# Performance work log

Hardware: AMD Instinct MI355X
Metric: run time of the kernel (lower is better)

The kernel has to match this reference:

```python
import jax, jax.numpy as jnp
import numpy as np

B, T, C = 2, 2048, 2048
NH, HS = 16, 128          # heads, head_size = C // NH
NLQ, NLKV = 512, 512      # q / kv latent dims
DHR = 64                  # decoupled rope head dim


def _rope_cos_sin(T, dhr, dtype=jnp.float32):
    inv = 1.0 / (10000.0 ** (np.arange(0, dhr, 2, dtype=np.float32) / dhr))
    ang = np.arange(T, dtype=np.float32)[:, None] * inv[None, :]  # [T, dhr//2]
    return jnp.asarray(np.cos(ang), dtype), jnp.asarray(np.sin(ang), dtype)


def setup_inputs() -> dict:
    key = jax.random.key(0)
    ks = jax.random.split(key, 10)
    s = 0.02
    cos, sin = _rope_cos_sin(T, DHR)
    return {
        "x":     jax.random.normal(ks[0], (B, T, C), jnp.float32),
        "cos":   cos,
        "sin":   sin,
        "W_dq":  s * jax.random.normal(ks[1], (NLQ, C), jnp.float32),
        "W_uq":  s * jax.random.normal(ks[2], (C, NLQ), jnp.float32),
        "W_dkv": s * jax.random.normal(ks[3], (NLKV, C), jnp.float32),
        "W_uk":  s * jax.random.normal(ks[4], (C, NLKV), jnp.float32),
        "W_uv":  s * jax.random.normal(ks[5], (C, NLKV), jnp.float32),
        "W_qr":  s * jax.random.normal(ks[6], (NH * DHR, NLQ), jnp.float32),
        "W_kr":  s * jax.random.normal(ks[7], (DHR, C), jnp.float32),
        "W_o":   s * jax.random.normal(ks[8], (C, C), jnp.float32),
    }


def _apply_rope(x, cos, sin):
    # x: [B, T, H, D]; pairs are interleaved (even=real, odd=imag)
    xr = x.reshape(x.shape[:-1] + (-1, 2))
    re, im = xr[..., 0], xr[..., 1]
    c = cos[None, :, None, :]
    s = sin[None, :, None, :]
    out = jnp.stack([re * c - im * s, re * s + im * c], axis=-1)
    return out.reshape(x.shape)


def reference(x, cos, sin, W_dq, W_uq, W_dkv, W_uk, W_uv, W_qr, W_kr, W_o):
    b, t, c = x.shape
    nh, hs, nlq, nlkv, dhr = NH, HS, NLQ, NLKV, DHR
    scale = 1.0 / np.sqrt(hs + dhr).astype(np.float32)

    # low-rank latents
    c_q = x @ W_dq.T          # [B, T, nlq]
    c_kv = x @ W_dkv.T        # [B, T, nlkv]

    # absorbed matrices (training path)
    # W_uq: [C, nlq] viewed as [nlq, nh, hs]; W_uk: [C, nlkv] viewed as [nh, hs, nlkv]
    k_eff = jnp.einsum('qhd,hdk->hqk', W_uq.reshape(nlq, nh, hs),
                       W_uk.reshape(nh, hs, nlkv))              # [nh, nlq, nlkv]
    v_eff = (W_uv.T @ W_o.T).reshape(nlkv, nh, hs).transpose(1, 0, 2)  # [nh, nlkv, hs]

    # content scores via absorbed low-rank path
    qk = jnp.einsum('btq,hqk->bhtk', c_q, k_eff)                # [B, nh, T, nlkv]
    attn_c = jnp.einsum('bhtk,bsk->bhts', qk, c_kv)             # [B, nh, T, T]

    # decoupled RoPE scores
    c_kr = (x @ W_kr.T)[:, :, None, :]                          # [B, T, 1, dhr]
    k_r = _apply_rope(c_kr, cos, sin)[:, :, 0, :]               # [B, T, dhr]
    c_qr = (c_q @ W_qr.T).reshape(b, t, nh, dhr)
    q_r = _apply_rope(c_qr, cos, sin)                            # [B, T, nh, dhr]
    attn_r = jnp.einsum('bthd,bsd->bhts', q_r, k_r)             # [B, nh, T, T]

    attn = (attn_c + attn_r) * scale
    mask = jnp.tril(jnp.ones((t, t), dtype=bool))
    attn = jnp.where(mask[None, None], attn, -jnp.inf)
    p = jax.nn.softmax(attn, axis=-1)

    ctx = jnp.einsum('bhts,bsk->bhtk', p, c_kv)                 # [B, nh, T, nlkv]
    y = jnp.einsum('bhtk,hkd->bthd', ctx, v_eff).reshape(b, t, c)
    return y
```

## Files before the change

kernel.cpp:

```cpp
#include <hip/hip_runtime.h>
#include <hip/hip_bf16.h>
#include <math.h>

typedef long long ll;
typedef unsigned short ushort_t;
typedef __attribute__((ext_vector_type(8))) __bf16 bf16x8;
typedef __attribute__((ext_vector_type(4))) float f32x4;

__device__ __forceinline__ ushort_t f2bf(float f) {
    __hip_bfloat16 h = __float2bfloat16(f);
    return *reinterpret_cast<ushort_t*>(&h);
}
__device__ __forceinline__ float bf2f(ushort_t u) {
    return __uint_as_float(((unsigned)u) << 16);
}
__device__ __forceinline__ void stage16(const void* g_lane, void* lds_uniform) {
    __builtin_amdgcn_global_load_lds(
        (const __attribute__((address_space(1))) unsigned int*)g_lane,
        (__attribute__((address_space(3))) unsigned int*)lds_uniform, 16, 0, 0);
}

#define DPPMAX(v, ctrl) v = fmaxf(v, __uint_as_float((unsigned)__builtin_amdgcn_update_dpp( \
        0, (int)__float_as_uint(v), (ctrl), 0xF, 0xF, true)))
#define DPPADD(v, ctrl) v = v + __uint_as_float((unsigned)__builtin_amdgcn_update_dpp( \
        0, (int)__float_as_uint(v), (ctrl), 0xF, 0xF, true))
__device__ __forceinline__ float red_max16(float v) {
    DPPMAX(v, 0xB1); DPPMAX(v, 0x4E); DPPMAX(v, 0x141); DPPMAX(v, 0x140); return v;
}
__device__ __forceinline__ float red_sum16(float v) {
    DPPADD(v, 0xB1); DPPADD(v, 0x4E); DPPADD(v, 0x141); DPPADD(v, 0x140); return v;
}

#define TM 128
#define TN 128
#define TK 64

__global__ __launch_bounds__(256)
void gemm_bf16(const ushort_t* __restrict__ Ab, const ushort_t* __restrict__ Bb,
               void* __restrict__ Cb,
               int M, int N, int K,
               int a_rs, int b_rs, int c_rs, int Z2,
               ll a_bs1, ll a_bs2, ll b_bs1, ll b_bs2, ll c_bs1, ll c_bs2,
               int out_f32)
{
    const int m0 = blockIdx.y * TM;
    const int n0 = blockIdx.x * TN;
    const int z1 = blockIdx.z / Z2, z2 = blockIdx.z % Z2;

    const ushort_t* A = Ab + z1 * a_bs1 + z2 * a_bs2;
    const ushort_t* B = Bb + z1 * b_bs1 + z2 * b_bs2;

    __shared__ ushort_t As[2][TM][TK];
    __shared__ ushort_t Bs[2][TN][TK];

    const int tid  = threadIdx.x;
    const int w    = tid >> 6;
    const int l    = tid & 63;
    const int lo16 = l & 15;
    const int quad = l >> 4;
    const int wm0  = (w & 1) * 64;
    const int wn0  = (w >> 1) * 64;

    const int srow  = l >> 3;
    const int sunit = (l & 7) ^ srow;

    f32x4 acc[4][4];
    const f32x4 zero = {0.f, 0.f, 0.f, 0.f};
#pragma unroll
    for (int mi = 0; mi < 4; ++mi)
#pragma unroll
        for (int nj = 0; nj < 4; ++nj) acc[mi][nj] = zero;

    const int nIter = K / TK;

#pragma unroll
    for (int i = 0; i < 4; ++i) {
        const int rr = w * 32 + i * 8;
        stage16(A + (ll)(m0 + rr + srow) * a_rs + sunit * 8, &As[0][rr][0]);
        stage16(B + (ll)(n0 + rr + srow) * b_rs + sunit * 8, &Bs[0][rr][0]);
    }

    int buf = 0;
    for (int it = 0; it < nIter; ++it) {
        __syncthreads();
        if (it + 1 < nIter) {
            const int k0 = (it + 1) * TK;
            const int nb = buf ^ 1;
#pragma unroll
            for (int i = 0; i < 4; ++i) {
                const int rr = w * 32 + i * 8;
                stage16(A + (ll)(m0 + rr + srow) * a_rs + (k0 + sunit * 8), &As[nb][rr][0]);
                stage16(B + (ll)(n0 + rr + srow) * b_rs + (k0 + sunit * 8), &Bs[nb][rr][0]);
            }
        }
#pragma unroll
        for (int h = 0; h < 2; ++h) {
            const int phys = (h * 4 + quad) ^ (lo16 & 7);
            bf16x8 af[4], bfr[4];
#pragma unroll
            for (int mi = 0; mi < 4; ++mi)
                af[mi] = *(const bf16x8*)&As[buf][wm0 + mi * 16 + lo16][phys * 8];
#pragma unroll
            for (int nj = 0; nj < 4; ++nj)
                bfr[nj] = *(const bf16x8*)&Bs[buf][wn0 + nj * 16 + lo16][phys * 8];
#pragma unroll
            for (int mi = 0; mi < 4; ++mi)
#pragma unroll
                for (int nj = 0; nj < 4; ++nj)
                    acc[mi][nj] = __builtin_amdgcn_mfma_f32_16x16x32_bf16(
                        af[mi], bfr[nj], acc[mi][nj], 0, 0, 0);
        }
        buf ^= 1;
    }

    if (out_f32) {
        float* C = (float*)Cb + z1 * c_bs1 + z2 * c_bs2;
#pragma unroll
        for (int mi = 0; mi < 4; ++mi)
#pragma unroll
            for (int r = 0; r < 4; ++r) {
                const ll row = m0 + wm0 + mi * 16 + quad * 4 + r;
                float* cr = C + row * (ll)c_rs + (n0 + wn0 + lo16);
#pragma unroll
                for (int nj = 0; nj < 4; ++nj) cr[nj * 16] = acc[mi][nj][r];
            }
    } else {
        ushort_t* C = (ushort_t*)Cb + z1 * c_bs1 + z2 * c_bs2;
#pragma unroll
        for (int mi = 0; mi < 4; ++mi)
#pragma unroll
            for (int r = 0; r < 4; ++r) {
                const ll row = m0 + wm0 + mi * 16 + quad * 4 + r;
                ushort_t* cr = C + row * (ll)c_rs + (n0 + wn0 + lo16);
#pragma unroll
                for (int nj = 0; nj < 4; ++nj) cr[nj * 16] = f2bf(acc[mi][nj][r]);
            }
    }
}

__global__ __launch_bounds__(256)
void prep_all(const float* __restrict__ x,    const float* __restrict__ Wo,
              const float* __restrict__ Wdq,  const float* __restrict__ Wdkv,
              const float* __restrict__ Wkr,  const float* __restrict__ Wuk,
              const float* __restrict__ Wuv,  const float* __restrict__ Wuq,
              const float* __restrict__ Wqr,
              ushort_t* __restrict__ xb,   ushort_t* __restrict__ Wo_b,
              ushort_t* __restrict__ WB1,  ushort_t* __restrict__ WukT,
              ushort_t* __restrict__ WuvT, ushort_t* __restrict__ WB2)
{
    __shared__ float tile[32][33];
    int bid = blockIdx.x;
    const int tid = threadIdx.x;

    if (bid < 8192) {
        ll i = (ll)bid * 256 + tid;
        float4 v = *(const float4*)(x + i * 4);
        ushort4 u;
        u.x = f2bf(v.x); u.y = f2bf(v.y); u.z = f2bf(v.z); u.w = f2bf(v.w);
        *(ushort4*)(xb + i * 4) = u;
        return;
    }
    bid -= 8192;
    if (bid < 4096) {
        ll i = (ll)bid * 256 + tid;
        float4 v = *(const float4*)(Wo + i * 4);
        ushort4 u;
        u.x = f2bf(v.x); u.y = f2bf(v.y); u.z = f2bf(v.z); u.w = f2bf(v.w);
        *(ushort4*)(Wo_b + i * 4) = u;
        return;
    }
    bid -= 4096;
    if (bid < 2304) {
        ll i4 = ((ll)bid * 256 + tid) * 4;
        int row = (int)(i4 >> 11);
        int col = (int)(i4 & 2047);
        float4 v = make_float4(0.f, 0.f, 0.f, 0.f);
        if (row < 512)       v = *(const float4*)(Wdq + (ll)row * 2048 + col);
        else if (row < 1024) v = *(const float4*)(Wdkv + (ll)(row - 512) * 2048 + col);
        else if (row < 1088) v = *(const float4*)(Wkr + (ll)(row - 1024) * 2048 + col);
        ushort4 u;
        u.x = f2bf(v.x); u.y = f2bf(v.y); u.z = f2bf(v.z); u.w = f2bf(v.w);
        *(ushort4*)(WB1 + i4) = u;
        return;
    }
    bid -= 2304;
    if (bid < 512) {
        ll i = (ll)bid * 256 + tid;
        float4 v = *(const float4*)(Wqr + i * 4);
        ushort4 u;
        u.x = f2bf(v.x); u.y = f2bf(v.y); u.z = f2bf(v.z); u.w = f2bf(v.w);
        *(ushort4*)(WB2 + (ll)2048 * 512 + i * 4) = u;
        return;
    }
    bid -= 512;

    const float* I; ushort_t* O; int R, C, r0, c0;
    if (bid < 1024) {
        int bx = bid & 15, by = (bid >> 4) & 3, bz = bid >> 6;
        I = Wuk + (ll)bz * 65536; O = WukT + (ll)bz * 65536;
        R = 128; C = 512; r0 = by * 32; c0 = bx * 32;
    } else if (bid < 2048) {
        int b2 = bid - 1024;
        I = Wuv; O = WuvT; R = 2048; C = 512;
        r0 = (b2 >> 4) * 32; c0 = (b2 & 15) * 32;
    } else {
        int b2 = bid - 2048;
        I = Wuq; O = WB2; R = 512; C = 2048;
        r0 = (b2 >> 6) * 32; c0 = (b2 & 63) * 32;
    }
    int tx = tid & 31, ty = tid >> 5;
#pragma unroll
    for (int i = 0; i < 4; ++i)
        tile[ty + i * 8][tx] = I[(ll)(r0 + ty + i * 8) * C + (c0 + tx)];
    __syncthreads();
#pragma unroll
    for (int i = 0; i < 4; ++i)
        O[(ll)(c0 + ty + i * 8) * R + (r0 + tx)] = f2bf(tile[tx][ty + i * 8]);
}

__global__ __launch_bounds__(256)
void reduce_veff(const float* __restrict__ s, ushort_t* __restrict__ out)
{
    ll i = ((ll)blockIdx.x * 256 + threadIdx.x) * 4;
    float4 a = *(const float4*)(s + i);
    float4 b = *(const float4*)(s + 1048576 + i);
    float4 c = *(const float4*)(s + 2097152 + i);
    float4 d = *(const float4*)(s + 3145728 + i);
    ushort4 u;
    u.x = f2bf(a.x + b.x + c.x + d.x);
    u.y = f2bf(a.y + b.y + c.y + d.y);
    u.z = f2bf(a.z + b.z + c.z + d.z);
    u.w = f2bf(a.w + b.w + c.w + d.w);
    *(ushort4*)(out + i) = u;
}

#define QP_RS 3072
#define XP_RS 1152

__global__ __launch_bounds__(512)
void flash_mla(const ushort_t* __restrict__ QP,
               const ushort_t* __restrict__ WukT,
               const ushort_t* __restrict__ XP,
               const ushort_t* __restrict__ VT,
               float* __restrict__ out,
               float scale)
{
    const int h  = blockIdx.y;
    const int b  = blockIdx.z;

    __shared__ __align__(16) char smem[98304];
    ushort_t* Q3 = (ushort_t*)(smem + 16384);

    const int tid  = threadIdx.x;
    const int w    = tid >> 6;
    const int g    = w >> 2;
    const int wl   = w & 3;
    const int l    = tid & 63;
    const int lo16 = l & 15;
    const int quad = l >> 4;
    char* Pw = smem + 90112 + w * 1024;

#pragma unroll 1
    for (int task = 0; task < 2; ++task) {
        const int jj = task ? (int)blockIdx.x : 15 - (int)blockIdx.x;
        const int qt = 2 * jj + g;
        const int t0 = qt * 64;
        const int nst = 4 * jj + 4;
        const int myLast = 2 * qt + (wl >> 1);

        __syncthreads();

        bf16x8 qa[18];

#pragma unroll
        for (int i = 0; i < 2; ++i) {
            int p = w * 128 + i * 64 + l;
            int r = p >> 4, u = p & 15, ul = u ^ (r & 15);
            stage16(WukT + ((ll)h * 512 + r) * 128 + ul * 8,
                    smem + 36864 + (ll)(w * 128 + i * 64) * 16);
        }
        bf16x8 ab[4];
#pragma unroll
        for (int kd = 0; kd < 4; ++kd)
            ab[kd] = *(const bf16x8*)(QP + (ll)(b * 2048 + t0 + 16 * wl + lo16) * QP_RS +
                                      h * 128 + kd * 32 + quad * 8);
        __syncthreads();

        int bwb = 0;
        for (int kc = 0; kc < 8; ++kc) {
            if (kc < 7) {
                char* bwn = smem + 36864 + (ll)(bwb ^ 1) * 16384;
#pragma unroll
                for (int i = 0; i < 2; ++i) {
                    int p = w * 128 + i * 64 + l;
                    int r = p >> 4, u = p & 15, ul = u ^ (r & 15);
                    stage16(WukT + ((ll)h * 512 + (kc + 1) * 64 + r) * 128 + ul * 8,
                            bwn + (ll)(w * 128 + i * 64) * 16);
                }
            }
            const ushort_t* BwC = (const ushort_t*)(smem + 36864 + (ll)bwb * 16384);
#pragma unroll
            for (int nt = 0; nt < 4; ++nt) {
                f32x4 c = {0.f, 0.f, 0.f, 0.f};
#pragma unroll
                for (int kd = 0; kd < 4; ++kd) {
                    bf16x8 bb = *(const bf16x8*)(BwC + (nt * 16 + lo16) * 128 +
                                                 (((kd * 4 + quad) ^ lo16) & 15) * 8);
                    c = __builtin_amdgcn_mfma_f32_16x16x32_bf16(ab[kd], bb, c, 0, 0, 0);
                }
#pragma unroll
                for (int r = 0; r < 4; ++r)
                    Q3[(w * 16 + quad * 4 + r) * 72 + nt * 16 + lo16] = f2bf(c[r]);
            }
#pragma unroll
            for (int kd2 = 0; kd2 < 2; ++kd2)
                qa[kc * 2 + kd2] = *(const bf16x8*)(Q3 + (w * 16 + lo16) * 72 + kd2 * 32 + quad * 8);

            __syncthreads();
            bwb ^= 1;
        }
#pragma unroll
        for (int kt = 16; kt < 18; ++kt)
            qa[kt] = *(const bf16x8*)(QP + (ll)(b * 2048 + t0 + 16 * wl + lo16) * QP_RS +
                                      2048 + h * 64 + (kt - 16) * 32 + quad * 8);

        f32x4 oacc[8];
        const f32x4 zero = {0.f, 0.f, 0.f, 0.f};
#pragma unroll
        for (int dt = 0; dt < 8; ++dt) oacc[dt] = zero;
        float mrow[4], lrow[4];
#pragma unroll
        for (int r = 0; r < 4; ++r) { mrow[r] = -3.0e38f; lrow[r] = 0.f; }

        if (w < 6) {
#pragma unroll
            for (int i = 0; i < 6; ++i) {
                int p = w * 384 + i * 64 + l;
                int r = p / 72, u = p % 72, ul = u ^ (r & 7);
                stage16(XP + (ll)(b * 2048 + r) * XP_RS + 512 + ul * 8,
                        smem + (ll)(w * 384 + i * 64) * 16);
            }
        } else {
#pragma unroll
            for (int i = 0; i < 4; ++i) {
                int p = (w - 6) * 256 + i * 64 + l;
                int r = p >> 2, u = p & 3, ul = u ^ (r & 3);
                stage16(VT + ((ll)(b * 16 + h) * 128 + r) * 2048 + ul * 8,
                        smem + 73728 + (ll)((w - 6) * 256 + i * 64) * 16);
            }
        }

        int buf = 0;
        for (int st = 0; st < nst; ++st) {
            __syncthreads();

            if (st + 1 < nst) {
                const int s0n = (st + 1) * 32;
                const int nb = buf ^ 1;
                if (w < 6) {
                    char* ksn = smem + nb * 36864;
#pragma unroll
                    for (int i = 0; i < 6; ++i) {
                        int p = w * 384 + i * 64 + l;
                        int r = p / 72, u = p % 72, ul = u ^ (r & 7);
                        stage16(XP + (ll)(b * 2048 + s0n + r) * XP_RS + 512 + ul * 8,
                                ksn + (ll)(w * 384 + i * 64) * 16);
                    }
                } else {
                    char* vsn = smem + 73728 + nb * 8192;
#pragma unroll
                    for (int i = 0; i < 4; ++i) {
                        int p = (w - 6) * 256 + i * 64 + l;
                        int r = p >> 2, u = p & 3, ul = u ^ (r & 3);
                        stage16(VT + ((ll)(b * 16 + h) * 128 + r) * 2048 + s0n + ul * 8,
                                vsn + (ll)((w - 6) * 256 + i * 64) * 16);
                    }
                }
            }

            if (st <= myLast) {
                const int s0 = st * 32;
                const ushort_t* Ks = (const ushort_t*)(smem + buf * 36864);
                const ushort_t* Vs = (const ushort_t*)(smem + 73728 + buf * 8192);

                f32x4 sc[2];
                sc[0] = zero; sc[1] = zero;
                __builtin_amdgcn_s_setprio(1);
#pragma unroll
                for (int kt = 0; kt < 18; ++kt)
#pragma unroll
                    for (int nt = 0; nt < 2; ++nt) {
                        int phys = (kt * 4 + quad) ^ (lo16 & 7);
                        bf16x8 kb = *(const bf16x8*)(Ks + (nt * 16 + lo16) * 576 + phys * 8);
                        sc[nt] = __builtin_amdgcn_mfma_f32_16x16x32_bf16(qa[kt], kb, sc[nt], 0, 0, 0);
                    }
                __builtin_amdgcn_s_setprio(0);

                const int rbase = 16 * wl + quad * 4;
#pragma unroll
                for (int nt = 0; nt < 2; ++nt)
#pragma unroll
                    for (int r = 0; r < 4; ++r) sc[nt][r] *= scale;
                if (st >= 2 * qt) {
#pragma unroll
                    for (int nt = 0; nt < 2; ++nt)
#pragma unroll
                        for (int r = 0; r < 4; ++r)
                            if ((s0 + nt * 16 + lo16) > (t0 + rbase + r))
                                sc[nt][r] = -INFINITY;
                }

                float alpha[4];
#pragma unroll
                for (int r = 0; r < 4; ++r) {
                    float tm = red_max16(fmaxf(sc[0][r], sc[1][r]));
                    float mnew = fmaxf(mrow[r], tm);
                    alpha[r] = __expf(mrow[r] - mnew);
                    mrow[r] = mnew;
                    sc[0][r] = __expf(sc[0][r] - mnew);
                    sc[1][r] = __expf(sc[1][r] - mnew);
                    float rs = red_sum16(sc[0][r] + sc[1][r]);
                    lrow[r] = lrow[r] * alpha[r] + rs;
                }
#pragma unroll
                for (int dt = 0; dt < 8; ++dt)
#pragma unroll
                    for (int r = 0; r < 4; ++r) oacc[dt][r] *= alpha[r];

#pragma unroll
                for (int nt = 0; nt < 2; ++nt)
#pragma unroll
                    for (int r = 0; r < 4; ++r) {
                        int row = quad * 4 + r;
                        int col = nt * 16 + lo16;
                        *(ushort_t*)(Pw + row * 64 + (((col >> 3) ^ (row & 3)) << 4) + (col & 7) * 2)
                            = f2bf(sc[nt][r]);
                    }
                bf16x8 pf = *(const bf16x8*)(Pw + lo16 * 64 + (quad ^ (lo16 & 3)) * 16);

                __builtin_amdgcn_s_setprio(1);
#pragma unroll
                for (int dt = 0; dt < 8; ++dt) {
                    int phys = quad ^ (lo16 & 3);
                    bf16x8 vb = *(const bf16x8*)(Vs + (dt * 16 + lo16) * 32 + phys * 8);
                    oacc[dt] = __builtin_amdgcn_mfma_f32_16x16x32_bf16(pf, vb, oacc[dt], 0, 0, 0);
                }
                __builtin_amdgcn_s_setprio(0);
            }
            buf ^= 1;
        }

#pragma unroll
        for (int r = 0; r < 4; ++r) {
            const float inv = 1.0f / lrow[r];
            const ll row = (ll)(b * 2048 + t0 + 16 * wl + quad * 4 + r);
#pragma unroll
            for (int dt = 0; dt < 8; ++dt)
                out[row * 2048 + h * 128 + dt * 16 + lo16] = oacc[dt][r] * inv;
        }
    }
}

__global__ void rope_kr(ushort_t* __restrict__ XP, const float* __restrict__ cb,
                        const float* __restrict__ sb)
{
    int idx = blockIdx.x * 256 + threadIdx.x;
    if (idx >= 2 * 2048 * 32) return;
    int j = idx & 31, t = (idx >> 5) & 2047, b = idx >> 16;
    float c = cb[t * 32 + j], s = sb[t * 32 + j];
    ushort_t* p = XP + ((ll)(b * 2048 + t)) * 1152 + 1024 + 2 * j;
    float re = bf2f(p[0]), im = bf2f(p[1]);
    p[0] = f2bf(re * c - im * s);
    p[1] = f2bf(re * s + im * c);
}

__global__ void rope_qr_ip(ushort_t* __restrict__ QP, const float* __restrict__ cb,
                           const float* __restrict__ sb)
{
    int idx = blockIdx.x * 256 + threadIdx.x;
    if (idx >= 4096 * 512) return;
    int pj = idx & 511, h = pj >> 5, j = pj & 31;
    int row = idx >> 9;
    int t = row & 2047;
    float c = cb[t * 32 + j], s = sb[t * 32 + j];
    ll base = (ll)row * 3072 + 2048 + h * 64 + 2 * j;
    float re = bf2f(QP[base]), im = bf2f(QP[base + 1]);
    QP[base]     = f2bf(re * c - im * s);
    QP[base + 1] = f2bf(re * s + im * c);
}

static inline void gemmb(hipStream_t st, const ushort_t* A, const ushort_t* B, void* C,
                         int M, int N, int K, int a_rs, int b_rs, int c_rs,
                         int nb, int Z2,
                         ll a_bs1, ll a_bs2, ll b_bs1, ll b_bs2, ll c_bs1, ll c_bs2,
                         int of32)
{
    dim3 g(N / TN, M / TM, nb);
    gemm_bf16<<<g, 256, 0, st>>>(A, B, C, M, N, K, a_rs, b_rs, c_rs, Z2,
                                 a_bs1, a_bs2, b_bs1, b_bs2, c_bs1, c_bs2, of32);
}

extern "C" void kernel_launch(void* const* d_in, const int* in_sizes, int n_in,
                              void* d_out, int out_size, void* d_ws, size_t ws_size,
                              hipStream_t stream)
{
    const float* x     = (const float*)d_in[0];
    const float* cosb  = (const float*)d_in[1];
    const float* sinb  = (const float*)d_in[2];
    const float* W_dq  = (const float*)d_in[3];
    const float* W_uq  = (const float*)d_in[4];
    const float* W_dkv = (const float*)d_in[5];
    const float* W_uk  = (const float*)d_in[6];
    const float* W_uv  = (const float*)d_in[7];
    const float* W_qr  = (const float*)d_in[8];
    const float* W_kr  = (const float*)d_in[9];
    const float* W_o   = (const float*)d_in[10];
    float* out = (float*)d_out;

    const float scale = 0.07216878364870323f;

    char* base = (char*)d_ws;
    ushort_t* WB1     = (ushort_t*)(base + 0);
    ushort_t* WukT_b  = (ushort_t*)(base + 4718592);
    ushort_t* WuvT_b  = (ushort_t*)(base + 6815744);
    ushort_t* WB2     = (ushort_t*)(base + 8912896);
    ushort_t* veffT_b = (ushort_t*)(base + 12058624);
    ushort_t* Wo_b    = (ushort_t*)(base + 14155776);
    ushort_t* xb      = (ushort_t*)(base + 22544384);
    ushort_t* XP      = (ushort_t*)(base + 39321600);
    ushort_t* VT_all  = (ushort_t*)(base + 48758784);
    ushort_t* QP      = (ushort_t*)(base + 65536000);
    float*    VTscr   = (float*)(base + 48758784);

    prep_all<<<18176, 256, 0, stream>>>(x, W_o, W_dq, W_dkv, W_kr, W_uk, W_uv, W_uq,
                                        W_qr, xb, Wo_b, WB1, WukT_b, WuvT_b, WB2);

    gemmb(stream, Wo_b, WuvT_b, VTscr, 128, 512, 512, 2048, 2048, 512,
          64, 16, 512, 262144, 512, 0, 1048576, 65536, 1);
    reduce_veff<<<1024, 256, 0, stream>>>(VTscr, veffT_b);

    gemmb(stream, xb, WB1, XP, 4096, 1152, 2048, 2048, 2048, 1152,
          1, 1, 0, 0, 0, 0, 0, 0, 0);
    rope_kr<<<512, 256, 0, stream>>>(XP, cosb, sinb);

    gemmb(stream, veffT_b, XP + 512, VT_all, 128, 2048, 512, 512, 1152, 2048,
          32, 16, 0, 65536, (ll)2048 * 1152, 0, (ll)16 * 262144, 262144, 0);

    gemmb(stream, XP, WB2, QP, 4096, 3072, 512, 1152, 512, 3072,
          1, 1, 0, 0, 0, 0, 0, 0, 0);
    rope_qr_ip<<<8192, 256, 0, stream>>>(QP, cosb, sinb);

    flash_mla<<<dim3(8, 16, 2), 512, 0, stream>>>(QP, WukT_b, XP, VT_all, out, scale);

    (void)in_sizes; (void)n_in; (void)out_size; (void)ws_size;
}
```

Before: 412.6 us.

## Fuse query RoPE into flash_mla and single-buffer the W_uk staging

Removes the standalone rope_qr_ip kernel and applies the rotary embedding to the q_r fragments as they are loaded in flash_mla, reading cos/sin directly. This removes one launch and a read-modify-write pass over the rope part of QP. The W_uk staging buffer for the absorbed-query GEMM moves to a single buffer at the start of shared memory, with barriers around each refill. This gives up the overlap of global loads with MFMA work, and a barrier is added before the later X/V staging that reuses the region.

```diff
diff --git a/kernel.cpp b/kernel.cpp
--- a/kernel.cpp
+++ b/kernel.cpp
@@ -242,6 +242,8 @@
                const ushort_t* __restrict__ WukT,
                const ushort_t* __restrict__ XP,
                const ushort_t* __restrict__ VT,
+               const float* __restrict__ cb,
+               const float* __restrict__ sb,
                float* __restrict__ out,
                float scale)
 {
@@ -249,6 +251,7 @@
     const int b  = blockIdx.z;
 
     __shared__ __align__(16) char smem[98304];
+    ushort_t* Bw = (ushort_t*)smem;
     ushort_t* Q3 = (ushort_t*)(smem + 16384);
 
     const int tid  = threadIdx.x;
@@ -277,7 +280,7 @@
             int p = w * 128 + i * 64 + l;
             int r = p >> 4, u = p & 15, ul = u ^ (r & 15);
             stage16(WukT + ((ll)h * 512 + r) * 128 + ul * 8,
-                    smem + 36864 + (ll)(w * 128 + i * 64) * 16);
+                    (char*)Bw + (ll)(w * 128 + i * 64) * 16);
         }
         bf16x8 ab[4];
 #pragma unroll
@@ -286,43 +289,57 @@
                                       h * 128 + kd * 32 + quad * 8);
         __syncthreads();
 
-        int bwb = 0;
         for (int kc = 0; kc < 8; ++kc) {
+#pragma unroll
+            for (int nt = 0; nt < 4; ++nt) {
+                f32x4 c = {0.f, 0.f, 0.f, 0.f};
+#pragma unroll
+                for (int kd = 0; kd < 4; ++kd) {
+                    bf16x8 bb = *(const bf16x8*)(Bw + (nt * 16 + lo16) * 128 +
+                                                 (((kd * 4 + quad) ^ lo16) & 15) * 8);
+                    c = __builtin_amdgcn_mfma_f32_16x16x32_bf16(ab[kd], bb, c, 0, 0, 0);
+                }
+#pragma unroll
+                for (int r = 0; r < 4; ++r)
+                    Q3[(w * 16 + quad * 4 + r) * 72 + nt * 16 + lo16] = f2bf(c[r]);
+            }
+#pragma unroll
+            for (int kd2 = 0; kd2 < 2; ++kd2)
+                qa[kc * 2 + kd2] = *(const bf16x8*)(Q3 + (w * 16 + lo16) * 72 + kd2 * 32 + quad * 8);
+
             if (kc < 7) {
-                char* bwn = smem + 36864 + (ll)(bwb ^ 1) * 16384;
+                __syncthreads();
 #pragma unroll
                 for (int i = 0; i < 2; ++i) {
                     int p = w * 128 + i * 64 + l;
                     int r = p >> 4, u = p & 15, ul = u ^ (r & 15);
                     stage16(WukT + ((ll)h * 512 + (kc + 1) * 64 + r) * 128 + ul * 8,
-                            bwn + (ll)(w * 128 + i * 64) * 16);
-                }
-            }
-            const ushort_t* BwC = (const ushort_t*)(smem + 36864 + (ll)bwb * 16384);
-#pragma unroll
-            for (int nt = 0; nt < 4; ++nt) {
-                f32x4 c = {0.f, 0.f, 0.f, 0.f};
-#pragma unroll
-                for (int kd = 0; kd < 4; ++kd) {
-                    bf16x8 bb = *(const bf16x8*)(BwC + (nt * 16 + lo16) * 128 +
-                                                 (((kd * 4 + quad) ^ lo16) & 15) * 8);
-                    c = __builtin_amdgcn_mfma_f32_16x16x32_bf16(ab[kd], bb, c, 0, 0, 0);
-                }
-#pragma unroll
-                for (int r = 0; r < 4; ++r)
-                    Q3[(w * 16 + quad * 4 + r) * 72 + nt * 16 + lo16] = f2bf(c[r]);
-            }
-#pragma unroll
-            for (int kd2 = 0; kd2 < 2; ++kd2)
-                qa[kc * 2 + kd2] = *(const bf16x8*)(Q3 + (w * 16 + lo16) * 72 + kd2 * 32 + quad * 8);
-
-            __syncthreads();
-            bwb ^= 1;
-        }
-#pragma unroll
-        for (int kt = 16; kt < 18; ++kt)
-            qa[kt] = *(const bf16x8*)(QP + (ll)(b * 2048 + t0 + 16 * wl + lo16) * QP_RS +
-                                      2048 + h * 64 + (kt - 16) * 32 + quad * 8);
+                            (char*)Bw + (ll)(w * 128 + i * 64) * 16);
+                }
+                __syncthreads();
+            }
+        }
+        {
+            const int t = t0 + 16 * wl + lo16;
+#pragma unroll
+            for (int kt = 16; kt < 18; ++kt) {
+                bf16x8 q = *(const bf16x8*)(QP + (ll)(b * 2048 + t) * QP_RS +
+                                            2048 + h * 64 + (kt - 16) * 32 + quad * 8);
+                const int j0 = (kt - 16) * 16 + quad * 4;
+                float4 c4 = *(const float4*)(cb + t * 32 + j0);
+                float4 s4 = *(const float4*)(sb + t * 32 + j0);
+                float cv[4] = {c4.x, c4.y, c4.z, c4.w};
+                float sv[4] = {s4.x, s4.y, s4.z, s4.w};
+                ushort_t tw[8];
+#pragma unroll
+                for (int p2 = 0; p2 < 4; ++p2) {
+                    float re = (float)q[2 * p2], im = (float)q[2 * p2 + 1];
+                    tw[2 * p2]     = f2bf(re * cv[p2] - im * sv[p2]);
+                    tw[2 * p2 + 1] = f2bf(re * sv[p2] + im * cv[p2]);
+                }
+                qa[kt] = *(const bf16x8*)tw;
+            }
+        }
 
         f32x4 oacc[8];
         const f32x4 zero = {0.f, 0.f, 0.f, 0.f};
@@ -331,6 +348,8 @@
         float mrow[4], lrow[4];
 #pragma unroll
         for (int r = 0; r < 4; ++r) { mrow[r] = -3.0e38f; lrow[r] = 0.f; }
+
+        __syncthreads();
 
         if (w < 6) {
 #pragma unroll
@@ -472,21 +491,6 @@
     float re = bf2f(p[0]), im = bf2f(p[1]);
     p[0] = f2bf(re * c - im * s);
     p[1] = f2bf(re * s + im * c);
-}
-
-__global__ void rope_qr_ip(ushort_t* __restrict__ QP, const float* __restrict__ cb,
-                           const float* __restrict__ sb)
-{
-    int idx = blockIdx.x * 256 + threadIdx.x;
-    if (idx >= 4096 * 512) return;
-    int pj = idx & 511, h = pj >> 5, j = pj & 31;
-    int row = idx >> 9;
-    int t = row & 2047;
-    float c = cb[t * 32 + j], s = sb[t * 32 + j];
-    ll base = (ll)row * 3072 + 2048 + h * 64 + 2 * j;
-    float re = bf2f(QP[base]), im = bf2f(QP[base + 1]);
-    QP[base]     = f2bf(re * c - im * s);
-    QP[base + 1] = f2bf(re * s + im * c);
 }
 
 static inline void gemmb(hipStream_t st, const ushort_t* A, const ushort_t* B, void* C,
@@ -548,9 +552,9 @@
 
     gemmb(stream, XP, WB2, QP, 4096, 3072, 512, 1152, 512, 3072,
           1, 1, 0, 0, 0, 0, 0, 0, 0);
-    rope_qr_ip<<<8192, 256, 0, stream>>>(QP, cosb, sinb);
-
-    flash_mla<<<dim3(8, 16, 2), 512, 0, stream>>>(QP, WukT_b, XP, VT_all, out, scale);
+
+    flash_mla<<<dim3(8, 16, 2), 512, 0, stream>>>(QP, WukT_b, XP, VT_all,
+                                                  cosb, sinb, out, scale);
 
     (void)in_sizes; (void)n_in; (void)out_size; (void)ws_size;
 }
```

Result: slower. 421.1 us (+2.1%).
